# Kernel optimization log

Measured on AMD Instinct MI355X. Metric: run time of the kernel, lower is better.

## Reference

```python
import jax, jax.numpy as jnp
import numpy as np

N_ATOMS = 204800
NUM_GRAPHS = 4096
NUM_STEMS = 81920   # 20 stems per graph
NUM_JBONDS = 40960  # 10 jbonds per graph
DIM = 128
NUM_OUT_PER_STEM = 105


def setup_inputs() -> dict:
    key = jax.random.key(0)
    ks = jax.random.split(key, 8)
    s = 1.0 / np.sqrt(DIM)
    return {
        "per_atom_out": jax.random.normal(ks[0], (N_ATOMS, DIM), jnp.float32),
        "scalar_outs": jax.random.normal(ks[1], (NUM_GRAPHS, 2), jnp.float32),
        "stem_atmidx": jax.random.randint(ks[2], (NUM_STEMS,), 0, N_ATOMS),
        "jbond_atmidx": jax.random.randint(ks[3], (NUM_JBONDS, 2), 0, N_ATOMS),
        "num_graphs": NUM_GRAPHS,
        "W1s": jax.random.normal(ks[4], (DIM, DIM), jnp.float32) * s,
        "b1s": jnp.zeros((DIM,), jnp.float32),
        "W2s": jax.random.normal(ks[5], (DIM, NUM_OUT_PER_STEM), jnp.float32) * s,
        "b2s": jnp.zeros((NUM_OUT_PER_STEM,), jnp.float32),
        "W1j": jax.random.normal(ks[6], (DIM, DIM), jnp.float32) * s,
        "b1j": jnp.zeros((DIM,), jnp.float32),
        "W2j": jax.random.normal(ks[7], (DIM, 1), jnp.float32) * s,
        "b2j": jnp.zeros((1,), jnp.float32),
    }


def _mlp(x, W1, b1, W2, b2):
    h = jax.nn.leaky_relu(x @ W1 + b1, negative_slope=0.01)
    return h @ W2 + b2


def reference(per_atom_out, scalar_outs, stem_atmidx, jbond_atmidx, num_graphs,
              W1s, b1s, W2s, b2s, W1j, b1j, W2j, b2j):
    # Gather per-stem atom features, run stem MLP: [num_stems, 105]
    stem_preds = _mlp(per_atom_out[stem_atmidx], W1s, b1s, W2s, b2s)
    # Gather both atoms of each jbond, run jbond MLP, mean over the 2 atoms
    jb = _mlp(per_atom_out[jbond_atmidx.reshape(-1)], W1j, b1j, W2j, b2j)  # [num_jbonds*2, 1]
    jbond_preds = jb.reshape(jbond_atmidx.shape).mean(axis=1)  # [num_jbonds]

    stop_logit = scalar_outs[:, 1:2]                       # [G, 1]
    break_logits = jbond_preds.reshape((num_graphs, -1))   # [G, jbonds_per_graph]
    add_logits = stem_preds.reshape((num_graphs, -1))      # [G, stems_per_graph*105]
    actor_logits = jnp.concatenate([stop_logit, break_logits, add_logits], axis=1)
    value = scalar_outs[:, :1]
    return (value, actor_logits)
```

## Files before the change

### kernel.cpp

```cpp
#include <hip/hip_runtime.h>

#define DIM 128
#define NGRAPH 4096
#define NSTEM 81920
#define NJROW 81920
#define NOUT 105
#define COLS 2111
#define SPG 20
#define ROWS 64
#define XPAD 136
#define NBS 640
#define NBJ 640

typedef __attribute__((ext_vector_type(8))) short bf16x8;
typedef __attribute__((ext_vector_type(4))) float f32x4;

__device__ __forceinline__ unsigned short f2bf(float f) {
    unsigned int u = __builtin_bit_cast(unsigned int, f);
    return (unsigned short)((u + 0x7fffu + ((u >> 16) & 1u)) >> 16);
}
__device__ __forceinline__ unsigned int pk2(float x, float y) {
    return ((unsigned int)f2bf(y) << 16) | f2bf(x);
}
__device__ __forceinline__ float lrelu(float v) { return v > 0.f ? v : 0.01f * v; }

__global__ __launch_bounds__(256) void prep_kernel(
    const float* __restrict__ W1s, const float* __restrict__ W2s,
    const float* __restrict__ W1j, const float* __restrict__ so,
    short* __restrict__ ws, float* __restrict__ out)
{
    int b = blockIdx.x;
    if (b < 24) {
        int mat = b >> 3, rg = b & 7;
        const float* W; short* dst; int NT, N;
        if (mat == 0)      { W = W1s; dst = ws;         NT = 8; N = 128; }
        else if (mat == 1) { W = W2s; dst = ws + 16384; NT = 7; N = 105; }
        else               { W = W1j; dst = ws + 30720; NT = 8; N = 128; }
        int Npad = NT * 16;
        int r2 = threadIdx.x >> 7;
        int n  = threadIdx.x & 127;
        #pragma unroll
        for (int rr = 0; rr < 16; rr += 2) {
            int k = rg * 16 + rr + r2;
            if (n < Npad) {
                float v = (n < N) ? W[k * N + n] : 0.f;
                int kt = k >> 5, i = k & 7, sub = (k >> 3) & 3;
                int lane = sub * 16 + (n & 15), nt = n >> 4;
                dst[((kt * NT + nt) * 64 + lane) * 8 + i] = (short)f2bf(v);
            }
        }
    } else {
        int g = (b - 24) * 256 + threadIdx.x;
        if (g < NGRAPH) {
            float2 v = *(const float2*)(so + 2 * g);
            out[g] = v.x;
            out[NGRAPH + g * COLS] = v.y;
        }
    }
}

__device__ __forceinline__ void mfma_layer(const short (*X)[XPAD],
                                           const bf16x8 (&wf)[4][2],
                                           int lc, int lq, f32x4 (&acc)[4][2])
{
    #pragma unroll
    for (int kt = 0; kt < 4; ++kt) {
        bf16x8 A0 = *(const bf16x8*)&X[lc]     [kt * 32 + lq * 8];
        bf16x8 A1 = *(const bf16x8*)&X[16 + lc][kt * 32 + lq * 8];
        bf16x8 A2 = *(const bf16x8*)&X[32 + lc][kt * 32 + lq * 8];
        bf16x8 A3 = *(const bf16x8*)&X[48 + lc][kt * 32 + lq * 8];
        #pragma unroll
        for (int j = 0; j < 2; ++j) {
            acc[0][j] = __builtin_amdgcn_mfma_f32_16x16x32_bf16(A0, wf[kt][j], acc[0][j], 0, 0, 0);
            acc[1][j] = __builtin_amdgcn_mfma_f32_16x16x32_bf16(A1, wf[kt][j], acc[1][j], 0, 0, 0);
            acc[2][j] = __builtin_amdgcn_mfma_f32_16x16x32_bf16(A2, wf[kt][j], acc[2][j], 0, 0, 0);
            acc[3][j] = __builtin_amdgcn_mfma_f32_16x16x32_bf16(A3, wf[kt][j], acc[3][j], 0, 0, 0);
        }
    }
}

__device__ __forceinline__ void stage_lds(short (*X)[XPAD], int rb, int ko,
                                          const float4* g)
{
    #pragma unroll
    for (int q = 0; q < 4; ++q) {
        uint4 p;
        p.x = pk2(g[2*q].x, g[2*q].y);     p.y = pk2(g[2*q].z, g[2*q].w);
        p.z = pk2(g[2*q+1].x, g[2*q+1].y); p.w = pk2(g[2*q+1].z, g[2*q+1].w);
        *(uint4*)&X[q * 16 + rb][ko] = p;
    }
}

__global__ __launch_bounds__(256, 2) void fused_mlp(
    const float* __restrict__ atom,
    const int* __restrict__ sidx, const int* __restrict__ jidx,
    const short* __restrict__ wsp,
    const float* __restrict__ b1s, const float* __restrict__ b2s,
    const float* __restrict__ b1j,
    const float* __restrict__ W2j, const float* __restrict__ b2j,
    float* __restrict__ out)
{
    __shared__ short Xs[2][ROWS][XPAD];
    __shared__ float red[4][ROWS];
    const int tid = threadIdx.x;
    const bool isStem = blockIdx.x < NBS;
    const int pb = isStem ? blockIdx.x : blockIdx.x - NBS;
    const int w = tid >> 6, l = tid & 63;
    const int lq = l >> 4, lc = l & 15;
    const int rb = tid >> 4, ko = (tid & 15) * 8;

    const int*   idx = isStem ? sidx : jidx;
    const short* W1p = isStem ? wsp : wsp + 30720;
    const float* b1  = isStem ? b1s : b1j;
    const int base0 = pb * 2 * ROWS;
    const int base1 = base0 + ROWS;

    int a0[4], a1[4];
    #pragma unroll
    for (int q = 0; q < 4; ++q) { a0[q] = idx[base0 + q * 16 + rb]; a1[q] = idx[base1 + q * 16 + rb]; }

    float4 g0[8], g1[8];
    #pragma unroll
    for (int q = 0; q < 4; ++q) {
        g0[2*q]   = *(const float4*)(atom + a0[q] * DIM + ko);
        g0[2*q+1] = *(const float4*)(atom + a0[q] * DIM + ko + 4);
    }
    #pragma unroll
    for (int q = 0; q < 4; ++q) {
        g1[2*q]   = *(const float4*)(atom + a1[q] * DIM + ko);
        g1[2*q+1] = *(const float4*)(atom + a1[q] * DIM + ko + 4);
    }

    bf16x8 wf1[4][2];
    #pragma unroll
    for (int kt = 0; kt < 4; ++kt)
        #pragma unroll
        for (int j = 0; j < 2; ++j)
            wf1[kt][j] = *(const bf16x8*)(W1p + ((kt * 8 + w * 2 + j) * 64 + l) * 8);
    float bb1[2];
    #pragma unroll
    for (int j = 0; j < 2; ++j) bb1[j] = b1[(w * 2 + j) * 16 + lc];

    bf16x8 wf2[4][2];
    float bb2[2];
    float wv0 = 0.f, wv1 = 0.f, bj = 0.f;
    if (isStem) {
        const short* W2p = wsp + 16384;
        #pragma unroll
        for (int kt = 0; kt < 4; ++kt)
            #pragma unroll
            for (int j = 0; j < 2; ++j) {
                int nt = w * 2 + j; if (nt > 6) nt = 6;
                wf2[kt][j] = *(const bf16x8*)(W2p + ((kt * 7 + nt) * 64 + l) * 8);
            }
        #pragma unroll
        for (int j = 0; j < 2; ++j) {
            int c = (w * 2 + j) * 16 + lc;
            bb2[j] = (c < NOUT) ? b2s[c] : 0.f;
        }
    } else {
        wv0 = W2j[(w * 2) * 16 + lc];
        wv1 = W2j[(w * 2 + 1) * 16 + lc];
        bj  = b2j[0];
    }

    stage_lds(Xs[0], rb, ko, g0);
    __syncthreads();

    if (isStem) {
        #pragma unroll
        for (int tt = 0; tt < 2; ++tt) {
            f32x4 acc[4][2];
            #pragma unroll
            for (int j = 0; j < 2; ++j)
                #pragma unroll
                for (int m = 0; m < 4; ++m)
                    acc[m][j] = (f32x4){bb1[j], bb1[j], bb1[j], bb1[j]};
            mfma_layer(Xs[tt], wf1, lc, lq, acc);
            if (tt == 0) stage_lds(Xs[1], rb, ko, g1);
            __syncthreads();
            #pragma unroll
            for (int j = 0; j < 2; ++j)
                #pragma unroll
                for (int m = 0; m < 4; ++m)
                    #pragma unroll
                    for (int rg = 0; rg < 4; ++rg)
                        Xs[tt][m * 16 + lq * 4 + rg][(w * 2 + j) * 16 + lc] =
                            (short)f2bf(lrelu(acc[m][j][rg]));
            __syncthreads();

            f32x4 acc2[4][2];
            #pragma unroll
            for (int j = 0; j < 2; ++j)
                #pragma unroll
                for (int m = 0; m < 4; ++m)
                    acc2[m][j] = (f32x4){bb2[j], bb2[j], bb2[j], bb2[j]};
            mfma_layer(Xs[tt], wf2, lc, lq, acc2);

            const int baseS = base0 + tt * ROWS;
            #pragma unroll
            for (int m = 0; m < 4; ++m)
                #pragma unroll
                for (int rg = 0; rg < 4; ++rg) {
                    int S = baseS + m * 16 + lq * 4 + rg;
                    int gph = S / SPG, sl = S - gph * SPG;
                    float* ob = out + NGRAPH + gph * COLS + 1 + 10 + sl * NOUT;
                    #pragma unroll
                    for (int j = 0; j < 2; ++j) {
                        int c = (w * 2 + j) * 16 + lc;
                        if (c < NOUT) ob[c] = acc2[m][j][rg];
                    }
                }
        }
    } else {
        #pragma unroll
        for (int tt = 0; tt < 2; ++tt) {
            f32x4 acc[4][2];
            #pragma unroll
            for (int j = 0; j < 2; ++j)
                #pragma unroll
                for (int m = 0; m < 4; ++m)
                    acc[m][j] = (f32x4){bb1[j], bb1[j], bb1[j], bb1[j]};
            mfma_layer(Xs[tt], wf1, lc, lq, acc);
            if (tt == 0) stage_lds(Xs[1], rb, ko, g1);

            float pf[4][4];
            #pragma unroll
            for (int m = 0; m < 4; ++m)
                #pragma unroll
                for (int rg = 0; rg < 4; ++rg)
                    pf[m][rg] = lrelu(acc[m][0][rg]) * wv0 + lrelu(acc[m][1][rg]) * wv1;
            #pragma unroll
            for (int off = 1; off < 16; off <<= 1)
                #pragma unroll
                for (int m = 0; m < 4; ++m)
                    #pragma unroll
                    for (int rg = 0; rg < 4; ++rg)
                        pf[m][rg] += __shfl_xor(pf[m][rg], off, 64);
            if (lc == 0)
                #pragma unroll
                for (int m = 0; m < 4; ++m)
                    #pragma unroll
                    for (int rg = 0; rg < 4; ++rg)
                        red[w][m * 16 + lq * 4 + rg] = pf[m][rg];
            __syncthreads();
            if (tid < 32) {
                int r0 = tid * 2;
                float s0 = red[0][r0] + red[1][r0] + red[2][r0] + red[3][r0];
                float s1 = red[0][r0+1] + red[1][r0+1] + red[2][r0+1] + red[3][r0+1];
                float v = (s0 + s1) * 0.5f + bj;
                int B = (pb * 2 + tt) * 32 + tid;
                int g = B / 10, c = B - g * 10;
                out[NGRAPH + g * COLS + 1 + c] = v;
            }
            __syncthreads();
        }
    }
}

extern "C" void kernel_launch(void* const* d_in, const int* in_sizes, int n_in,
                              void* d_out, int out_size, void* d_ws, size_t ws_size,
                              hipStream_t stream) {
    const float* per_atom_out = (const float*)d_in[0];
    const float* scalar_outs  = (const float*)d_in[1];
    const int*   stem_atmidx  = (const int*)d_in[2];
    const int*   jbond_atmidx = (const int*)d_in[3];
    const float* W1s = (const float*)d_in[5];
    const float* b1s = (const float*)d_in[6];
    const float* W2s = (const float*)d_in[7];
    const float* b2s = (const float*)d_in[8];
    const float* W1j = (const float*)d_in[9];
    const float* b1j = (const float*)d_in[10];
    const float* W2j = (const float*)d_in[11];
    const float* b2j = (const float*)d_in[12];
    float* out = (float*)d_out;
    short* wsp = (short*)d_ws;

    hipLaunchKernelGGL(prep_kernel, dim3(40), dim3(256), 0, stream,
                       W1s, W2s, W1j, scalar_outs, wsp, out);
    hipLaunchKernelGGL(fused_mlp, dim3(NBS + NBJ), dim3(256), 0, stream,
                       per_atom_out, stem_atmidx, jbond_atmidx, wsp,
                       b1s, b2s, b1j, W2j, b2j, out);
}
```

Before: 40.20 us.

## Process four row tiles per block with a software-pipelined gather and separate hidden buffer

Each block now handles four 64-row tiles instead of two and launches half as many blocks. The gather for the next tile is issued into registers before the current tile's MFMA work and staged into a double-buffered LDS tile afterwards. The hidden activations move to a dedicated LDS buffer so layer 2 no longer overwrites the input tile. The aim is to hide gather latency behind compute and amortise weight-fragment loads, at the cost of 640 blocks (fewer than before) for latency hiding and more LDS per block.

Result: faster. 34.55 us (-14.0%).

```diff
diff --git a/kernel.cpp b/kernel.cpp
--- a/kernel.cpp
+++ b/kernel.cpp
@@ -9,8 +9,9 @@
 #define SPG 20
 #define ROWS 64
 #define XPAD 136
-#define NBS 640
-#define NBJ 640
+#define TT 4
+#define NBSB 320
+#define NBJB 320
 
 typedef __attribute__((ext_vector_type(8))) short bf16x8;
 typedef __attribute__((ext_vector_type(4))) float f32x4;
@@ -79,8 +80,18 @@
     }
 }
 
+__device__ __forceinline__ void issue_gather(const float* __restrict__ atom,
+                                             const int (&a)[4], int ko, float4 (&g)[8])
+{
+    #pragma unroll
+    for (int q = 0; q < 4; ++q) {
+        g[2*q]   = *(const float4*)(atom + a[q] * DIM + ko);
+        g[2*q+1] = *(const float4*)(atom + a[q] * DIM + ko + 4);
+    }
+}
+
 __device__ __forceinline__ void stage_lds(short (*X)[XPAD], int rb, int ko,
-                                          const float4* g)
+                                          const float4 (&g)[8])
 {
     #pragma unroll
     for (int q = 0; q < 4; ++q) {
@@ -100,11 +111,12 @@
     const float* __restrict__ W2j, const float* __restrict__ b2j,
     float* __restrict__ out)
 {
-    __shared__ short Xs[2][ROWS][XPAD];
+    __shared__ short Xbuf[2][ROWS][XPAD];
+    __shared__ short Hbuf[ROWS][XPAD];
     __shared__ float red[4][ROWS];
     const int tid = threadIdx.x;
-    const bool isStem = blockIdx.x < NBS;
-    const int pb = isStem ? blockIdx.x : blockIdx.x - NBS;
+    const bool isStem = blockIdx.x < NBSB;
+    const int pb = isStem ? blockIdx.x : blockIdx.x - NBSB;
     const int w = tid >> 6, l = tid & 63;
     const int lq = l >> 4, lc = l & 15;
     const int rb = tid >> 4, ko = (tid & 15) * 8;
@@ -112,24 +124,17 @@
     const int*   idx = isStem ? sidx : jidx;
     const short* W1p = isStem ? wsp : wsp + 30720;
     const float* b1  = isStem ? b1s : b1j;
-    const int base0 = pb * 2 * ROWS;
-    const int base1 = base0 + ROWS;
-
-    int a0[4], a1[4];
-    #pragma unroll
-    for (int q = 0; q < 4; ++q) { a0[q] = idx[base0 + q * 16 + rb]; a1[q] = idx[base1 + q * 16 + rb]; }
-
-    float4 g0[8], g1[8];
-    #pragma unroll
-    for (int q = 0; q < 4; ++q) {
-        g0[2*q]   = *(const float4*)(atom + a0[q] * DIM + ko);
-        g0[2*q+1] = *(const float4*)(atom + a0[q] * DIM + ko + 4);
-    }
-    #pragma unroll
-    for (int q = 0; q < 4; ++q) {
-        g1[2*q]   = *(const float4*)(atom + a1[q] * DIM + ko);
-        g1[2*q+1] = *(const float4*)(atom + a1[q] * DIM + ko + 4);
-    }
+    const int tbase = pb * TT * ROWS;
+
+    int a[TT][4];
+    #pragma unroll
+    for (int t = 0; t < TT; ++t)
+        #pragma unroll
+        for (int q = 0; q < 4; ++q)
+            a[t][q] = idx[tbase + t * ROWS + q * 16 + rb];
+
+    float4 g[8];
+    issue_gather(atom, a[0], ko, g);
 
     bf16x8 wf1[4][2];
     #pragma unroll
@@ -164,28 +169,29 @@
         bj  = b2j[0];
     }
 
-    stage_lds(Xs[0], rb, ko, g0);
+    stage_lds(Xbuf[0], rb, ko, g);
     __syncthreads();
 
     if (isStem) {
         #pragma unroll
-        for (int tt = 0; tt < 2; ++tt) {
+        for (int t = 0; t < TT; ++t) {
+            if (t + 1 < TT) issue_gather(atom, a[t + 1], ko, g);
+
             f32x4 acc[4][2];
             #pragma unroll
             for (int j = 0; j < 2; ++j)
                 #pragma unroll
                 for (int m = 0; m < 4; ++m)
                     acc[m][j] = (f32x4){bb1[j], bb1[j], bb1[j], bb1[j]};
-            mfma_layer(Xs[tt], wf1, lc, lq, acc);
-            if (tt == 0) stage_lds(Xs[1], rb, ko, g1);
-            __syncthreads();
+            mfma_layer(Xbuf[t & 1], wf1, lc, lq, acc);
+
             #pragma unroll
             for (int j = 0; j < 2; ++j)
                 #pragma unroll
                 for (int m = 0; m < 4; ++m)
                     #pragma unroll
                     for (int rg = 0; rg < 4; ++rg)
-                        Xs[tt][m * 16 + lq * 4 + rg][(w * 2 + j) * 16 + lc] =
+                        Hbuf[m * 16 + lq * 4 + rg][(w * 2 + j) * 16 + lc] =
                             (short)f2bf(lrelu(acc[m][j][rg]));
             __syncthreads();
 
@@ -195,9 +201,11 @@
                 #pragma unroll
                 for (int m = 0; m < 4; ++m)
                     acc2[m][j] = (f32x4){bb2[j], bb2[j], bb2[j], bb2[j]};
-            mfma_layer(Xs[tt], wf2, lc, lq, acc2);
-
-            const int baseS = base0 + tt * ROWS;
+            mfma_layer(Hbuf, wf2, lc, lq, acc2);
+
+            if (t + 1 < TT) stage_lds(Xbuf[(t + 1) & 1], rb, ko, g);
+
+            const int baseS = tbase + t * ROWS;
             #pragma unroll
             for (int m = 0; m < 4; ++m)
                 #pragma unroll
@@ -211,18 +219,20 @@
                         if (c < NOUT) ob[c] = acc2[m][j][rg];
                     }
                 }
+            __syncthreads();
         }
     } else {
         #pragma unroll
-        for (int tt = 0; tt < 2; ++tt) {
+        for (int t = 0; t < TT; ++t) {
+            if (t + 1 < TT) issue_gather(atom, a[t + 1], ko, g);
+
             f32x4 acc[4][2];
             #pragma unroll
             for (int j = 0; j < 2; ++j)
                 #pragma unroll
                 for (int m = 0; m < 4; ++m)
                     acc[m][j] = (f32x4){bb1[j], bb1[j], bb1[j], bb1[j]};
-            mfma_layer(Xs[tt], wf1, lc, lq, acc);
-            if (tt == 0) stage_lds(Xs[1], rb, ko, g1);
+            mfma_layer(Xbuf[t & 1], wf1, lc, lq, acc);
 
             float pf[4][4];
             #pragma unroll
@@ -244,15 +254,17 @@
                     for (int rg = 0; rg < 4; ++rg)
                         red[w][m * 16 + lq * 4 + rg] = pf[m][rg];
             __syncthreads();
+
             if (tid < 32) {
                 int r0 = tid * 2;
                 float s0 = red[0][r0] + red[1][r0] + red[2][r0] + red[3][r0];
                 float s1 = red[0][r0+1] + red[1][r0+1] + red[2][r0+1] + red[3][r0+1];
                 float v = (s0 + s1) * 0.5f + bj;
-                int B = (pb * 2 + tt) * 32 + tid;
-                int g = B / 10, c = B - g * 10;
-                out[NGRAPH + g * COLS + 1 + c] = v;
+                int B = (pb * TT + t) * 32 + tid;
+                int gg = B / 10, c = B - gg * 10;
+                out[NGRAPH + gg * COLS + 1 + c] = v;
             }
+            if (t + 1 < TT) stage_lds(Xbuf[(t + 1) & 1], rb, ko, g);
             __syncthreads();
         }
     }
@@ -278,7 +290,7 @@
 
     hipLaunchKernelGGL(prep_kernel, dim3(40), dim3(256), 0, stream,
                        W1s, W2s, W1j, scalar_outs, wsp, out);
-    hipLaunchKernelGGL(fused_mlp, dim3(NBS + NBJ), dim3(256), 0, stream,
+    hipLaunchKernelGGL(fused_mlp, dim3(NBSB + NBJB), dim3(256), 0, stream,
                        per_atom_out, stem_atmidx, jbond_atmidx, wsp,
                        b1s, b2s, b1j, W2j, b2j, out);
 }
```
